# Kernel tuning notes

Measured on AMD Instinct MI355X. Metric: run time of the kernel, lower is better.

Reference implementation:

```python
import jax, jax.numpy as jnp
import numpy as np

B, C, T = 16, 2048, 128      # batch, enc_in (variables), d_model
ID, NC, CD, GD, OUT = 32, 16, 32, 32, 96  # id_dim, num_clusters, cluster_dim, graph_dim, out_len
GIN = T + ID + CD            # gcn_input_dim = 192
NEG = -1.0e9


def setup_inputs() -> dict:
    key = jax.random.key(0)
    ks = jax.random.split(key, 13)
    s = 0.02
    return {
        "x": jax.random.normal(ks[0], (B, C, 1, T), dtype=jnp.float32),
        "id_emb": jax.random.normal(ks[1], (C, ID), dtype=jnp.float32) * s,
        "w1": jax.random.normal(ks[2], (T, T // 2), dtype=jnp.float32) * s,
        "b1": jnp.zeros((T // 2,), dtype=jnp.float32),
        "w2": jax.random.normal(ks[3], (T // 2, ID), dtype=jnp.float32) * s,
        "b2": jnp.zeros((ID,), dtype=jnp.float32),
        "cluster_emb": jax.random.normal(ks[4], (NC, CD), dtype=jnp.float32) * s,
        "wic": jax.random.normal(ks[5], (ID, CD), dtype=jnp.float32) * s,
        "bic": jnp.zeros((CD,), dtype=jnp.float32),
        "wg": jax.random.normal(ks[6], (ID + CD, GD), dtype=jnp.float32) * s,
        "bg": jnp.zeros((GD,), dtype=jnp.float32),
        "context_weight": jax.random.normal(ks[7], (C, GIN), dtype=jnp.float32) * s,
        "wl": jax.random.normal(ks[8], (GIN, OUT), dtype=jnp.float32) * s,
        "bl": jnp.zeros((OUT,), dtype=jnp.float32),
    }


def reference(x, id_emb, w1, b1, w2, b2, cluster_emb, wic, bic, wg, bg,
              context_weight, wl, bl):
    b, c, n, t = x.shape
    xs = x[:, :, 0, :]                                       # [b,c,t] (squeeze dim -2)
    # dynamic id projection: Linear -> ReLU -> Linear
    dyn = jax.nn.relu(xs @ w1 + b1) @ w2 + b2                # [b,c,id]
    id_embeds = id_emb[None, :, :] + dyn                     # static + dynamic
    # soft cluster assignment
    id_for_clustering = id_embeds @ wic + bic                # [b,c,cd]
    probs = jax.nn.softmax(
        jnp.einsum('bcl,nl->bcn', id_for_clustering, cluster_emb), axis=-1)
    cluster_embeds = probs @ cluster_emb                     # [b,c,cd]
    # graph embedding and dynamic dense adjacency
    graph_emb = jnp.concatenate([id_embeds, cluster_embeds], axis=-1) @ wg + bg
    adj = jnp.einsum('bcg,bmg->bcm', graph_emb, graph_emb)   # [b,c,c]
    adj = jax.nn.relu(adj)
    neg = NEG * jnp.eye(c, dtype=adj.dtype)                  # [c,c], -1e9 on diag, 0 off-diag
    adj = adj + neg
    # torch.where(adj<=0, neg_inf_matrix, adj): off-diag nonpositive -> 0, diag -> -1e9
    adj = jnp.where(adj <= 0.0, neg, adj)
    adj = jax.nn.softmax(adj, axis=-1)
    # two-stage GCN aggregation (dropout is identity in eval mode)
    gcn_input = jnp.concatenate([xs, id_embeds, cluster_embeds], axis=-1)  # [b,c,GIN]
    agg = jnp.einsum('boi,bid->bod', adj, gcn_input)         # [b,c,GIN]
    w = jnp.tanh(jnp.einsum('bod,ol->bdl', agg, context_weight))  # [b,GIN,GIN]
    out = (jnp.einsum('bdl,bod->bol', w, gcn_input) + gcn_input) @ wl + bl  # [b,c,out_len]
    return out[:, :, None, :]                                # unsqueeze dim -2
```

## Files before the change

kernel.cpp:

```cpp
#include <hip/hip_runtime.h>
#include <hip/hip_bf16.h>


typedef __attribute__((ext_vector_type(8))) short short8;
typedef __attribute__((ext_vector_type(16))) float f32x16;

__device__ __forceinline__ unsigned short f2bf(float f) {
    __hip_bfloat16 h = __float2bfloat16(f);
    return *reinterpret_cast<unsigned short*>(&h);
}
__device__ __forceinline__ float bf2f(unsigned short u) {
    __hip_bfloat16 h = *reinterpret_cast<__hip_bfloat16*>(&u);
    return __bfloat162float(h);
}

__global__ __launch_bounds__(256) void k0_transpose_x(
    const float* __restrict__ x, unsigned short* __restrict__ vt)
{
    __shared__ float sT[64 * 133];
    const int t = threadIdx.x;
    const int m0 = blockIdx.x * 64;
    const int b = blockIdx.y;
    const float* xb = x + (size_t)b * 2048 * 128;
    #pragma unroll
    for (int kk = 0; kk < 8; ++kk) {
        int i = t + kk * 256;
        int mm = i >> 5, q4 = i & 31;
        float4 v = ((const float4*)(xb + (size_t)(m0 + mm) * 128))[q4];
        float* d = sT + mm * 133 + q4 * 4;
        d[0] = v.x; d[1] = v.y; d[2] = v.z; d[3] = v.w;
    }
    __syncthreads();
    const int mp = t & 31;
    const int ch0 = t >> 5;
    #pragma unroll
    for (int pass = 0; pass < 16; ++pass) {
        int ch = ch0 + pass * 8;
        unsigned int u0 = f2bf(sT[(2 * mp) * 133 + ch]);
        unsigned int u1 = f2bf(sT[(2 * mp + 1) * 133 + ch]);
        *((unsigned int*)(vt + (size_t)(b * 192 + ch) * 2048 + m0) + mp) =
            u0 | (u1 << 16);
    }
}

__global__ __launch_bounds__(256) void k1_tiled(
    const float* __restrict__ x, const float* __restrict__ id_emb,
    const float* __restrict__ w1, const float* __restrict__ b1,
    const float* __restrict__ w2, const float* __restrict__ b2,
    const float* __restrict__ ce, const float* __restrict__ wic,
    const float* __restrict__ bic, const float* __restrict__ wg,
    const float* __restrict__ bg, unsigned short* __restrict__ vt,
    unsigned short* __restrict__ geb16)
{
    __shared__ float sh[32 * 68];
    __shared__ float sid[32 * 36];
    __shared__ float sic[32 * 36];
    __shared__ float scl[32 * 36];
    __shared__ float sp[32 * 20];

    const int t = threadIdx.x;
    const int r0 = blockIdx.x * 32;
    const int b = r0 >> 11;
    const int c0 = r0 & 2047;

    {
        const int row = t >> 3, j0 = (t & 7) * 8;
        const float* xrow = x + (size_t)(r0 + row) * 128;
        float acc[8];
        #pragma unroll
        for (int j = 0; j < 8; ++j) acc[j] = b1[j0 + j];
        float4 pa[4], pb[4];
        float4 pxv;
        #pragma unroll
        for (int u = 0; u < 4; ++u) {
            const float4* wr = (const float4*)(w1 + u * 64 + j0);
            pa[u] = wr[0]; pb[u] = wr[1];
        }
        pxv = *(const float4*)(xrow);
        for (int k0 = 0; k0 < 128; k0 += 4) {
            float4 ca[4], cb[4];
            float4 cxv = pxv;
            #pragma unroll
            for (int u = 0; u < 4; ++u) { ca[u] = pa[u]; cb[u] = pb[u]; }
            const int kn = k0 + 4;
            if (kn < 128) {
                #pragma unroll
                for (int u = 0; u < 4; ++u) {
                    const float4* wr = (const float4*)(w1 + (kn + u) * 64 + j0);
                    pa[u] = wr[0]; pb[u] = wr[1];
                }
                pxv = *(const float4*)(xrow + kn);
            }
            float cx[4] = {cxv.x, cxv.y, cxv.z, cxv.w};
            #pragma unroll
            for (int u = 0; u < 4; ++u) {
                acc[0] = fmaf(cx[u], ca[u].x, acc[0]);
                acc[1] = fmaf(cx[u], ca[u].y, acc[1]);
                acc[2] = fmaf(cx[u], ca[u].z, acc[2]);
                acc[3] = fmaf(cx[u], ca[u].w, acc[3]);
                acc[4] = fmaf(cx[u], cb[u].x, acc[4]);
                acc[5] = fmaf(cx[u], cb[u].y, acc[5]);
                acc[6] = fmaf(cx[u], cb[u].z, acc[6]);
                acc[7] = fmaf(cx[u], cb[u].w, acc[7]);
            }
        }
        float* hr = sh + row * 68 + j0;
        #pragma unroll
        for (int j = 0; j < 8; ++j) hr[j] = fmaxf(acc[j], 0.f);
    }
    __syncthreads();

    {
        const int row = t >> 3, j0 = (t & 7) * 4;
        const int c = c0 + row;
        const float* hrow = sh + row * 68;
        float acc[4];
        #pragma unroll
        for (int j = 0; j < 4; ++j) acc[j] = b2[j0 + j];
        float4 pw[4];
        float  ph[4];
        #pragma unroll
        for (int u = 0; u < 4; ++u) {
            pw[u] = *(const float4*)(w2 + u * 32 + j0);
            ph[u] = hrow[u];
        }
        for (int k0 = 0; k0 < 64; k0 += 4) {
            float4 cw4[4];
            float  ch4[4];
            #pragma unroll
            for (int u = 0; u < 4; ++u) { cw4[u] = pw[u]; ch4[u] = ph[u]; }
            const int kn = k0 + 4;
            if (kn < 64) {
                #pragma unroll
                for (int u = 0; u < 4; ++u) {
                    pw[u] = *(const float4*)(w2 + (kn + u) * 32 + j0);
                    ph[u] = hrow[kn + u];
                }
            }
            #pragma unroll
            for (int u = 0; u < 4; ++u) {
                acc[0] = fmaf(ch4[u], cw4[u].x, acc[0]);
                acc[1] = fmaf(ch4[u], cw4[u].y, acc[1]);
                acc[2] = fmaf(ch4[u], cw4[u].z, acc[2]);
                acc[3] = fmaf(ch4[u], cw4[u].w, acc[3]);
            }
        }
        #pragma unroll
        for (int j = 0; j < 4; ++j) {
            float ide = id_emb[c * 32 + j0 + j] + acc[j];
            sid[row * 36 + j0 + j] = ide;
            vt[(size_t)(b * 192 + 128 + j0 + j) * 2048 + c] = f2bf(ide);
        }
    }
    __syncthreads();

    {
        const int row = t >> 3, j0 = (t & 7) * 4;
        const float* irow = sid + row * 36;
        float acc[4];
        #pragma unroll
        for (int j = 0; j < 4; ++j) acc[j] = bic[j0 + j];
        float4 pw[4];
        float  pi[4];
        #pragma unroll
        for (int u = 0; u < 4; ++u) {
            pw[u] = *(const float4*)(wic + u * 32 + j0);
            pi[u] = irow[u];
        }
        for (int k0 = 0; k0 < 32; k0 += 4) {
            float4 cw4[4];
            float  ci4[4];
            #pragma unroll
            for (int u = 0; u < 4; ++u) { cw4[u] = pw[u]; ci4[u] = pi[u]; }
            const int kn = k0 + 4;
            if (kn < 32) {
                #pragma unroll
                for (int u = 0; u < 4; ++u) {
                    pw[u] = *(const float4*)(wic + (kn + u) * 32 + j0);
                    pi[u] = irow[kn + u];
                }
            }
            #pragma unroll
            for (int u = 0; u < 4; ++u) {
                acc[0] = fmaf(ci4[u], cw4[u].x, acc[0]);
                acc[1] = fmaf(ci4[u], cw4[u].y, acc[1]);
                acc[2] = fmaf(ci4[u], cw4[u].z, acc[2]);
                acc[3] = fmaf(ci4[u], cw4[u].w, acc[3]);
            }
        }
        #pragma unroll
        for (int j = 0; j < 4; ++j) sic[row * 36 + j0 + j] = acc[j];
    }
    __syncthreads();

    {
        const int n = t & 15, rowp = t >> 4;
        const float* cer = ce + n * 32;
        float a0 = 0.f, a1 = 0.f;
        #pragma unroll
        for (int k0 = 0; k0 < 32; k0 += 8) {
            float cv[8], s0[8], s1[8];
            #pragma unroll
            for (int u = 0; u < 8; ++u) {
                cv[u] = cer[k0 + u];
                s0[u] = sic[rowp * 36 + k0 + u];
                s1[u] = sic[(rowp + 16) * 36 + k0 + u];
            }
            #pragma unroll
            for (int u = 0; u < 8; ++u) {
                a0 = fmaf(s0[u], cv[u], a0);
                a1 = fmaf(s1[u], cv[u], a1);
            }
        }
        sp[rowp * 20 + n] = a0;
        sp[(rowp + 16) * 20 + n] = a1;
    }
    __syncthreads();

    if (t < 32) {
        float* pr = sp + t * 20;
        float mx = pr[0];
        for (int n = 1; n < 16; ++n) mx = fmaxf(mx, pr[n]);
        float ss = 0.f;
        for (int n = 0; n < 16; ++n) { float e = __expf(pr[n] - mx); pr[n] = e; ss += e; }
        float inv = 1.f / ss;
        for (int n = 0; n < 16; ++n) pr[n] *= inv;
    }
    __syncthreads();

    {
        const int row = t >> 3, j0 = (t & 7) * 4;
        const int c = c0 + row;
        const float* prow = sp + row * 20;
        float acc[4] = {0.f, 0.f, 0.f, 0.f};
        float4 pc[4];
        float  pp[4];
        #pragma unroll
        for (int u = 0; u < 4; ++u) {
            pc[u] = *(const float4*)(ce + u * 32 + j0);
            pp[u] = prow[u];
        }
        for (int n0 = 0; n0 < 16; n0 += 4) {
            float4 cc4[4];
            float  cp4[4];
            #pragma unroll
            for (int u = 0; u < 4; ++u) { cc4[u] = pc[u]; cp4[u] = pp[u]; }
            const int nn = n0 + 4;
            if (nn < 16) {
                #pragma unroll
                for (int u = 0; u < 4; ++u) {
                    pc[u] = *(const float4*)(ce + (nn + u) * 32 + j0);
                    pp[u] = prow[nn + u];
                }
            }
            #pragma unroll
            for (int u = 0; u < 4; ++u) {
                acc[0] = fmaf(cp4[u], cc4[u].x, acc[0]);
                acc[1] = fmaf(cp4[u], cc4[u].y, acc[1]);
                acc[2] = fmaf(cp4[u], cc4[u].z, acc[2]);
                acc[3] = fmaf(cp4[u], cc4[u].w, acc[3]);
            }
        }
        #pragma unroll
        for (int j = 0; j < 4; ++j) {
            scl[row * 36 + j0 + j] = acc[j];
            vt[(size_t)(b * 192 + 160 + j0 + j) * 2048 + c] = f2bf(acc[j]);
        }
    }
    __syncthreads();

    {
        const int row = t >> 3, j0 = (t & 7) * 4;
        const int r = r0 + row;
        const float* irow = sid + row * 36;
        const float* crow = scl + row * 36;
        float acc[4];
        #pragma unroll
        for (int j = 0; j < 4; ++j) acc[j] = bg[j0 + j];
        {
            float4 pw[4];
            float  pi[4];
            #pragma unroll
            for (int u = 0; u < 4; ++u) {
                pw[u] = *(const float4*)(wg + u * 32 + j0);
                pi[u] = irow[u];
            }
            for (int k0 = 0; k0 < 32; k0 += 4) {
                float4 cw4[4];
                float  ci4[4];
                #pragma unroll
                for (int u = 0; u < 4; ++u) { cw4[u] = pw[u]; ci4[u] = pi[u]; }
                const int kn = k0 + 4;
                if (kn < 32) {
                    #pragma unroll
                    for (int u = 0; u < 4; ++u) {
                        pw[u] = *(const float4*)(wg + (kn + u) * 32 + j0);
                        pi[u] = irow[kn + u];
                    }
                }
                #pragma unroll
                for (int u = 0; u < 4; ++u) {
                    acc[0] = fmaf(ci4[u], cw4[u].x, acc[0]);
                    acc[1] = fmaf(ci4[u], cw4[u].y, acc[1]);
                    acc[2] = fmaf(ci4[u], cw4[u].z, acc[2]);
                    acc[3] = fmaf(ci4[u], cw4[u].w, acc[3]);
                }
            }
        }
        {
            float4 pw[4];
            float  pcv[4];
            #pragma unroll
            for (int u = 0; u < 4; ++u) {
                pw[u] = *(const float4*)(wg + (32 + u) * 32 + j0);
                pcv[u] = crow[u];
            }
            for (int k0 = 0; k0 < 32; k0 += 4) {
                float4 cw4[4];
                float  cc4[4];
                #pragma unroll
                for (int u = 0; u < 4; ++u) { cw4[u] = pw[u]; cc4[u] = pcv[u]; }
                const int kn = k0 + 4;
                if (kn < 32) {
                    #pragma unroll
                    for (int u = 0; u < 4; ++u) {
                        pw[u] = *(const float4*)(wg + (32 + kn + u) * 32 + j0);
                        pcv[u] = crow[kn + u];
                    }
                }
                #pragma unroll
                for (int u = 0; u < 4; ++u) {
                    acc[0] = fmaf(cc4[u], cw4[u].x, acc[0]);
                    acc[1] = fmaf(cc4[u], cw4[u].y, acc[1]);
                    acc[2] = fmaf(cc4[u], cw4[u].z, acc[2]);
                    acc[3] = fmaf(cc4[u], cw4[u].w, acc[3]);
                }
            }
        }
        #pragma unroll
        for (int j = 0; j < 4; ++j)
            geb16[(size_t)r * 32 + j0 + j] = f2bf(acc[j]);
    }
}

__global__ __launch_bounds__(256) void k1b_sumv(
    const unsigned short* __restrict__ vt, float* __restrict__ sumv)
{
    __shared__ float red[256];
    const int ch = blockIdx.x, b = blockIdx.y, t = threadIdx.x;
    const unsigned short* row = vt + (size_t)(b * 192 + ch) * 2048;
    float a = 0.f;
    #pragma unroll
    for (int j = 0; j < 8; ++j) a += bf2f(row[t * 8 + j]);
    red[t] = a; __syncthreads();
    for (int off = 128; off > 0; off >>= 1) {
        if (t < off) red[t] += red[t + off];
        __syncthreads();
    }
    if (t == 0) sumv[b * 192 + ch] = red[0];
}

__global__ __launch_bounds__(256) void k2_fused(
    const unsigned short* __restrict__ geb16,
    const unsigned short* __restrict__ vt,
    const float* __restrict__ sumv,
    unsigned short* __restrict__ aggb)
{
    __shared__ unsigned short sGe[2][64 * 40];
    __shared__ unsigned short sVt[192 * 72];
    __shared__ unsigned short dw[64 * 72];
    __shared__ float s_sum[192];
    __shared__ float sinv[64];
    float* lpbuf = (float*)sVt;

    const int t = threadIdx.x;
    const int lin = blockIdx.x + gridDim.x * blockIdx.y;
    const int nb = (lin & 7) * 64 + (lin >> 3);
    const int o0 = (nb & 31) * 64;
    const int b = nb >> 5;
    const unsigned short* geb = geb16 + (size_t)b * 2048 * 32;
    const unsigned short* vtb = vt + (size_t)b * 192 * 2048;

    const int lane = t & 63;
    const int mg = t >> 6;
    const int col = lane & 31;
    const int grp = lane >> 5;
    const int os = (mg & 1) * 32;
    const int ms = (mg >> 1) * 32;
    const int orow0 = (mg & 1) * 32;
    const int dbase = (mg >> 1) * 96;

    const int ge_row = t >> 2, ge_c8 = t & 3;

    short8 rGe;
    short8 rVt0, rVt1, rVt2, rVt3, rVt4, rVt5;

    if (t < 192) s_sum[t] = sumv[b * 192 + t];

    short8 Areg0 = *(const short8*)(geb + (size_t)(o0 + os + col) * 32 + 0 * 16 + grp * 8);
    short8 Areg1 = *(const short8*)(geb + (size_t)(o0 + os + col) * 32 + 1 * 16 + grp * 8);

    {
        rGe = *(const short8*)(geb + (size_t)ge_row * 32 + ge_c8 * 8);
        int i0;
        i0 = t + 0 * 256; rVt0 = *(const short8*)(vtb + (size_t)(i0 >> 3) * 2048 + 0 + (i0 & 7) * 8);
        i0 = t + 1 * 256; rVt1 = *(const short8*)(vtb + (size_t)(i0 >> 3) * 2048 + 0 + (i0 & 7) * 8);
        i0 = t + 2 * 256; rVt2 = *(const short8*)(vtb + (size_t)(i0 >> 3) * 2048 + 0 + (i0 & 7) * 8);
        i0 = t + 3 * 256; rVt3 = *(const short8*)(vtb + (size_t)(i0 >> 3) * 2048 + 0 + (i0 & 7) * 8);
        i0 = t + 4 * 256; rVt4 = *(const short8*)(vtb + (size_t)(i0 >> 3) * 2048 + 0 + (i0 & 7) * 8);
        i0 = t + 5 * 256; rVt5 = *(const short8*)(vtb + (size_t)(i0 >> 3) * 2048 + 0 + (i0 & 7) * 8);
    }
    {
        *(short8*)(sGe[0] + ge_row * 40 + ge_c8 * 8) = rGe;
        int i0;
        i0 = t + 0 * 256; *(short8*)(sVt + (i0 >> 3) * 72 + (i0 & 7) * 8) = rVt0;
        i0 = t + 1 * 256; *(short8*)(sVt + (i0 >> 3) * 72 + (i0 & 7) * 8) = rVt1;
        i0 = t + 2 * 256; *(short8*)(sVt + (i0 >> 3) * 72 + (i0 & 7) * 8) = rVt2;
        i0 = t + 3 * 256; *(short8*)(sVt + (i0 >> 3) * 72 + (i0 & 7) * 8) = rVt3;
        i0 = t + 4 * 256; *(short8*)(sVt + (i0 >> 3) * 72 + (i0 & 7) * 8) = rVt4;
        i0 = t + 5 * 256; *(short8*)(sVt + (i0 >> 3) * 72 + (i0 & 7) * 8) = rVt5;
    }
    __syncthreads();

    f32x16 acc0, acc1, acc2;
    #pragma unroll
    for (int i = 0; i < 16; ++i) { acc0[i] = 0.f; acc1[i] = 0.f; acc2[i] = 0.f; }
    float lpA[16];
    #pragma unroll
    for (int i = 0; i < 16; ++i) lpA[i] = 0.f;

    int cur = 0;
    for (int m0 = 0; m0 < 2048; m0 += 64) {
        const bool have_next = (m0 + 64 < 2048);

        if (have_next) {
            const int mn = m0 + 64;
            rGe = *(const short8*)(geb + (size_t)(mn + ge_row) * 32 + ge_c8 * 8);
            int i0;
            i0 = t + 0 * 256; rVt0 = *(const short8*)(vtb + (size_t)(i0 >> 3) * 2048 + mn + (i0 & 7) * 8);
            i0 = t + 1 * 256; rVt1 = *(const short8*)(vtb + (size_t)(i0 >> 3) * 2048 + mn + (i0 & 7) * 8);
            i0 = t + 2 * 256; rVt2 = *(const short8*)(vtb + (size_t)(i0 >> 3) * 2048 + mn + (i0 & 7) * 8);
            i0 = t + 3 * 256; rVt3 = *(const short8*)(vtb + (size_t)(i0 >> 3) * 2048 + mn + (i0 & 7) * 8);
            i0 = t + 4 * 256; rVt4 = *(const short8*)(vtb + (size_t)(i0 >> 3) * 2048 + mn + (i0 & 7) * 8);
            i0 = t + 5 * 256; rVt5 = *(const short8*)(vtb + (size_t)(i0 >> 3) * 2048 + mn + (i0 & 7) * 8);
        }

        f32x16 sacc;
        #pragma unroll
        for (int i = 0; i < 16; ++i) sacc[i] = 0.f;
        {
            short8 Bf0 = *(const short8*)(sGe[cur] + (ms + col) * 40 + 0 * 16 + grp * 8);
            short8 Bf1 = *(const short8*)(sGe[cur] + (ms + col) * 40 + 1 * 16 + grp * 8);
            sacc = __builtin_amdgcn_mfma_f32_32x32x16_bf16(Areg0, Bf0, sacc, 0, 0, 0);
            sacc = __builtin_amdgcn_mfma_f32_32x32x16_bf16(Areg1, Bf1, sacc, 0, 0, 0);
        }
        {
            const int m_local = ms + col;
            if (m0 != o0) {
                #pragma unroll
                for (int r = 0; r < 16; ++r) {
                    int o_local = os + (r & 3) + 8 * (r >> 2) + 4 * grp;
                    float s = sacc[r];
                    float d = (s > 0.f) ? (__expf(s) - 1.f) : 0.f;
                    lpA[r] += d;
                    dw[o_local * 72 + m_local] = f2bf(d);
                }
            } else {
                const int gm = m0 + m_local;
                #pragma unroll
                for (int r = 0; r < 16; ++r) {
                    int o_local = os + (r & 3) + 8 * (r >> 2) + 4 * grp;
                    float s = sacc[r];
                    float d = (gm == o0 + o_local) ? -1.f
                            : ((s > 0.f) ? (__expf(s) - 1.f) : 0.f);
                    lpA[r] += d;
                    dw[o_local * 72 + m_local] = f2bf(d);
                }
            }
        }
        if (have_next)
            *(short8*)(sGe[cur ^ 1] + ge_row * 40 + ge_c8 * 8) = rGe;

        __syncthreads();

        #pragma unroll
        for (int ks = 0; ks < 4; ++ks) {
            short8 A  = *(const short8*)(dw + (orow0 + col) * 72 + ks * 16 + grp * 8);
            short8 B0 = *(const short8*)(sVt + (dbase + col) * 72 + ks * 16 + grp * 8);
            short8 B1v = *(const short8*)(sVt + (dbase + 32 + col) * 72 + ks * 16 + grp * 8);
            short8 B2v = *(const short8*)(sVt + (dbase + 64 + col) * 72 + ks * 16 + grp * 8);
            acc0 = __builtin_amdgcn_mfma_f32_32x32x16_bf16(A, B0, acc0, 0, 0, 0);
            acc1 = __builtin_amdgcn_mfma_f32_32x32x16_bf16(A, B1v, acc1, 0, 0, 0);
            acc2 = __builtin_amdgcn_mfma_f32_32x32x16_bf16(A, B2v, acc2, 0, 0, 0);
        }

        __syncthreads();

        if (have_next) {
            int i0;
            i0 = t + 0 * 256; *(short8*)(sVt + (i0 >> 3) * 72 + (i0 & 7) * 8) = rVt0;
            i0 = t + 1 * 256; *(short8*)(sVt + (i0 >> 3) * 72 + (i0 & 7) * 8) = rVt1;
            i0 = t + 2 * 256; *(short8*)(sVt + (i0 >> 3) * 72 + (i0 & 7) * 8) = rVt2;
            i0 = t + 3 * 256; *(short8*)(sVt + (i0 >> 3) * 72 + (i0 & 7) * 8) = rVt3;
            i0 = t + 4 * 256; *(short8*)(sVt + (i0 >> 3) * 72 + (i0 & 7) * 8) = rVt4;
            i0 = t + 5 * 256; *(short8*)(sVt + (i0 >> 3) * 72 + (i0 & 7) * 8) = rVt5;
        }
        cur ^= 1;
    }

    __syncthreads();
    {
        const int widx = mg >> 1;
        #pragma unroll
        for (int r = 0; r < 16; ++r) {
            int ol = os + (r & 3) + 8 * (r >> 2) + 4 * grp;
            lpbuf[(widx * 32 + col) * 68 + ol] = lpA[r];
        }
    }
    __syncthreads();
    if (t < 64) {
        float l = 2048.f;
        for (int i = 0; i < 64; ++i) l += lpbuf[i * 68 + t];
        sinv[t] = 1.f / l;
    }
    __syncthreads();

    {
        f32x16 av[3] = {acc0, acc1, acc2};
        unsigned short* ab = aggb + (size_t)b * 2048 * 192;
        #pragma unroll
        for (int n = 0; n < 3; ++n) {
            int chn = dbase + n * 32 + col;
            float sv = s_sum[chn];
            #pragma unroll
            for (int r = 0; r < 16; ++r) {
                int ol = orow0 + (r & 3) + 8 * (r >> 2) + 4 * grp;
                ab[(size_t)(o0 + ol) * 192 + chn] =
                    f2bf((sv + av[n][r]) * sinv[ol]);
            }
        }
    }
}

__global__ __launch_bounds__(256) void k3a_split(
    const float* __restrict__ cw, unsigned short* __restrict__ cwhi,
    unsigned short* __restrict__ cwlo)
{
    const int idx = blockIdx.x * 256 + threadIdx.x;
    float v = cw[idx];
    unsigned short h = f2bf(v);
    cwhi[idx] = h;
    cwlo[idx] = f2bf(v - bf2f(h));
}

__global__ __launch_bounds__(256) void k3_mfma_sk(
    const unsigned short* __restrict__ aggb,
    const unsigned short* __restrict__ cwhi,
    const unsigned short* __restrict__ cwlo,
    float* __restrict__ wpart)
{
    const int t = threadIdx.x;
    const int slot = blockIdx.z;
    const int b = slot >> 3;
    const int ks = slot & 7;
    const int d0 = blockIdx.x * 64;
    const int l0 = blockIdx.y * 64;
    const unsigned short* ab = aggb + (size_t)b * 2048 * 192;

    const int lane = t & 63;
    const int w = t >> 6;
    const int col = lane & 31;
    const int grp = lane >> 5;
    const int drow = d0 + (w & 1) * 32 + col;
    const int lrow = l0 + (w >> 1) * 32 + col;

    f32x16 acc;
    #pragma unroll
    for (int i = 0; i < 16; ++i) acc[i] = 0.f;

    const int obase = ks * 256;
    #pragma unroll 4
    for (int ostep = 0; ostep < 16; ++ostep) {
        const int ob = obase + ostep * 16 + grp * 8;
        short8 A, Bh, Bl;
        #pragma unroll
        for (int i = 0; i < 8; ++i) {
            const size_t ro = (size_t)(ob + i) * 192;
            A[i]  = (short)ab[ro + drow];
            Bh[i] = (short)cwhi[ro + lrow];
            Bl[i] = (short)cwlo[ro + lrow];
        }
        acc = __builtin_amdgcn_mfma_f32_32x32x16_bf16(A, Bh, acc, 0, 0, 0);
        acc = __builtin_amdgcn_mfma_f32_32x32x16_bf16(A, Bl, acc, 0, 0, 0);
    }

    float* wp = wpart + (size_t)slot * 36864;
    const int lcol = l0 + (w >> 1) * 32 + col;
    #pragma unroll
    for (int r = 0; r < 16; ++r) {
        int dl = d0 + (w & 1) * 32 + (r & 3) + 8 * (r >> 2) + 4 * grp;
        wp[(size_t)dl * 192 + lcol] = acc[r];
    }
}

__global__ __launch_bounds__(256) void k3_ctx_sk(
    const unsigned short* __restrict__ aggb, const float* __restrict__ cw,
    float* __restrict__ wpart)
{
    __shared__ float sA[64 * 68];
    __shared__ float sW[64 * 68];
    const int t = threadIdx.x;
    const int slot = blockIdx.z;
    const int b = slot >> 3;
    const int ks = slot & 7;
    const int d0 = blockIdx.x * 64;
    const int l0 = blockIdx.y * 64;
    const unsigned short* ab = aggb + (size_t)b * 2048 * 192;
    const int ti = t >> 4, tj = t & 15;
    float acc[4][4] = {{0.f}};

    for (int o0 = ks * 256; o0 < ks * 256 + 256; o0 += 64) {
        for (int i = t; i < 4096; i += 256) {
            int oo = i >> 6, dd = i & 63;
            sA[oo * 68 + dd] = bf2f(ab[(size_t)(o0 + oo) * 192 + d0 + dd]);
            sW[oo * 68 + dd] = cw[(size_t)(o0 + oo) * 192 + l0 + dd];
        }
        __syncthreads();
        for (int o = 0; o < 64; ++o) {
            const float* ap = sA + o * 68 + ti * 4;
            const float* wp = sW + o * 68 + tj * 4;
            float a0 = ap[0], a1 = ap[1], a2 = ap[2], a3 = ap[3];
            float w0 = wp[0], w1v = wp[1], w2v = wp[2], w3 = wp[3];
            acc[0][0] = fmaf(a0, w0, acc[0][0]); acc[0][1] = fmaf(a0, w1v, acc[0][1]);
            acc[0][2] = fmaf(a0, w2v, acc[0][2]); acc[0][3] = fmaf(a0, w3, acc[0][3]);
            acc[1][0] = fmaf(a1, w0, acc[1][0]); acc[1][1] = fmaf(a1, w1v, acc[1][1]);
            acc[1][2] = fmaf(a1, w2v, acc[1][2]); acc[1][3] = fmaf(a1, w3, acc[1][3]);
            acc[2][0] = fmaf(a2, w0, acc[2][0]); acc[2][1] = fmaf(a2, w1v, acc[2][1]);
            acc[2][2] = fmaf(a2, w2v, acc[2][2]); acc[2][3] = fmaf(a2, w3, acc[2][3]);
            acc[3][0] = fmaf(a3, w0, acc[3][0]); acc[3][1] = fmaf(a3, w1v, acc[3][1]);
            acc[3][2] = fmaf(a3, w2v, acc[3][2]); acc[3][3] = fmaf(a3, w3, acc[3][3]);
        }
        __syncthreads();
    }
    float* wp = wpart + (size_t)slot * 36864;
    #pragma unroll
    for (int i = 0; i < 4; ++i)
        #pragma unroll
        for (int j = 0; j < 4; ++j)
            wp[(d0 + ti * 4 + i) * 192 + l0 + tj * 4 + j] = acc[i][j];
}

__global__ __launch_bounds__(256) void k3r_reduce(
    const float* __restrict__ wpart, float* __restrict__ wraw)
{
    const int idx = blockIdx.x * 256 + threadIdx.x;
    const int b = blockIdx.y;
    const float* base = wpart + (size_t)b * 8 * 36864 + idx;
    float a = 0.f;
    #pragma unroll
    for (int ks = 0; ks < 8; ++ks) a += base[(size_t)ks * 36864];
    wraw[(size_t)b * 36864 + idx] = tanhf(a);
}

__global__ __launch_bounds__(256) void k3_ctx(
    const unsigned short* __restrict__ aggb, const float* __restrict__ cw,
    float* __restrict__ wraw)
{
    __shared__ float sA[64 * 68];
    __shared__ float sW[64 * 68];
    const int t = threadIdx.x;
    const int b = blockIdx.z;
    const int d0 = blockIdx.x * 64;
    const int l0 = blockIdx.y * 64;
    const unsigned short* ab = aggb + (size_t)b * 2048 * 192;
    const int ti = t >> 4, tj = t & 15;
    float acc[4][4] = {{0.f}};

    for (int o0 = 0; o0 < 2048; o0 += 64) {
        for (int i = t; i < 4096; i += 256) {
            int oo = i >> 6, dd = i & 63;
            sA[oo * 68 + dd] = bf2f(ab[(size_t)(o0 + oo) * 192 + d0 + dd]);
            sW[oo * 68 + dd] = cw[(size_t)(o0 + oo) * 192 + l0 + dd];
        }
        __syncthreads();
        for (int o = 0; o < 64; ++o) {
            const float* ap = sA + o * 68 + ti * 4;
            const float* wp = sW + o * 68 + tj * 4;
            float a0 = ap[0], a1 = ap[1], a2 = ap[2], a3 = ap[3];
            float w0 = wp[0], w1v = wp[1], w2v = wp[2], w3 = wp[3];
            acc[0][0] = fmaf(a0, w0, acc[0][0]); acc[0][1] = fmaf(a0, w1v, acc[0][1]);
            acc[0][2] = fmaf(a0, w2v, acc[0][2]); acc[0][3] = fmaf(a0, w3, acc[0][3]);
            acc[1][0] = fmaf(a1, w0, acc[1][0]); acc[1][1] = fmaf(a1, w1v, acc[1][1]);
            acc[1][2] = fmaf(a1, w2v, acc[1][2]); acc[1][3] = fmaf(a1, w3, acc[1][3]);
            acc[2][0] = fmaf(a2, w0, acc[2][0]); acc[2][1] = fmaf(a2, w1v, acc[2][1]);
            acc[2][2] = fmaf(a2, w2v, acc[2][2]); acc[2][3] = fmaf(a2, w3, acc[2][3]);
            acc[3][0] = fmaf(a3, w0, acc[3][0]); acc[3][1] = fmaf(a3, w1v, acc[3][1]);
            acc[3][2] = fmaf(a3, w2v, acc[3][2]); acc[3][3] = fmaf(a3, w3, acc[3][3]);
        }
        __syncthreads();
    }
    float* wb = wraw + (size_t)b * 36864;
    #pragma unroll
    for (int i = 0; i < 4; ++i)
        #pragma unroll
        for (int j = 0; j < 4; ++j)
            wb[(d0 + ti * 4 + i) * 192 + l0 + tj * 4 + j] = tanhf(acc[i][j]);
}

__global__ __launch_bounds__(192) void k3b_m2(
    const float* __restrict__ wmat, const float* __restrict__ wl,
    float* __restrict__ m2)
{
    const int t = threadIdx.x;
    const int b = blockIdx.y;
    const int d = blockIdx.x * 2 + (t / 96);
    const int l = t % 96;
    const float* wrow = wmat + (size_t)b * 36864 + d * 192;
    float acc = wl[d * 96 + l];
    float pa[8], pb[8];
    #pragma unroll
    for (int u = 0; u < 8; ++u) { pa[u] = wrow[u]; pb[u] = wl[u * 96 + l]; }
    for (int k0 = 0; k0 < 192; k0 += 8) {
        float ca[8], cb[8];
        #pragma unroll
        for (int u = 0; u < 8; ++u) { ca[u] = pa[u]; cb[u] = pb[u]; }
        const int kn = k0 + 8;
        if (kn < 192) {
            #pragma unroll
            for (int u = 0; u < 8; ++u) {
                pa[u] = wrow[kn + u];
                pb[u] = wl[(kn + u) * 96 + l];
            }
        }
        #pragma unroll
        for (int u = 0; u < 8; ++u) acc = fmaf(ca[u], cb[u], acc);
    }
    m2[(size_t)b * 18432 + d * 96 + l] = acc;
}

__global__ __launch_bounds__(192) void k4_tiled(
    const float* __restrict__ x, const unsigned short* __restrict__ vt,
    const float* __restrict__ m2, const float* __restrict__ bl,
    float* __restrict__ out)
{
    __shared__ float sm2[192 * 96];
    const int t = threadIdx.x;
    const int rblk = blockIdx.x;
    const int b = blockIdx.y;
    {
        const float4* src = (const float4*)(m2 + (size_t)b * 18432);
        float4* dst = (float4*)sm2;
        #pragma unroll
        for (int i = 0; i < 24; ++i) dst[t + i * 192] = src[t + i * 192];
    }
    __syncthreads();

    const int rg = t / 12;
    const int cg = t % 12;
    const int j0 = cg * 8;
    const int cloc = rblk * 64 + rg * 4;
    const int rr = b * 2048 + cloc;
    float acc[4][8];
    #pragma unroll
    for (int i = 0; i < 4; ++i)
        #pragma unroll
        for (int j = 0; j < 8; ++j) acc[i][j] = bl[j0 + j];

    for (int k0 = 0; k0 < 128; k0 += 8) {
        float rv[4][8];
        #pragma unroll
        for (int i = 0; i < 4; ++i) {
            const float4* xr = (const float4*)(x + (size_t)(rr + i) * 128 + k0);
            float4 a = xr[0], c4 = xr[1];
            rv[i][0] = a.x; rv[i][1] = a.y; rv[i][2] = a.z; rv[i][3] = a.w;
            rv[i][4] = c4.x; rv[i][5] = c4.y; rv[i][6] = c4.z; rv[i][7] = c4.w;
        }
        #pragma unroll
        for (int kk = 0; kk < 8; ++kk) {
            const float* mr = sm2 + (k0 + kk) * 96 + j0;
            float mv[8];
            #pragma unroll
            for (int j = 0; j < 8; ++j) mv[j] = mr[j];
            #pragma unroll
            for (int i = 0; i < 4; ++i)
                #pragma unroll
                for (int j = 0; j < 8; ++j)
                    acc[i][j] = fmaf(rv[i][kk], mv[j], acc[i][j]);
        }
    }
    for (int k = 128; k < 192; ++k) {
        const unsigned short* vr = vt + (size_t)(b * 192 + k) * 2048 + cloc;
        float rv0 = bf2f(vr[0]), rv1 = bf2f(vr[1]);
        float rv2 = bf2f(vr[2]), rv3 = bf2f(vr[3]);
        const float* mr = sm2 + k * 96 + j0;
        #pragma unroll
        for (int j = 0; j < 8; ++j) {
            float mv = mr[j];
            acc[0][j] = fmaf(rv0, mv, acc[0][j]);
            acc[1][j] = fmaf(rv1, mv, acc[1][j]);
            acc[2][j] = fmaf(rv2, mv, acc[2][j]);
            acc[3][j] = fmaf(rv3, mv, acc[3][j]);
        }
    }
    #pragma unroll
    for (int i = 0; i < 4; ++i) {
        float* orow = out + (size_t)(rr + i) * 96 + j0;
        *(float4*)orow = make_float4(acc[i][0], acc[i][1], acc[i][2], acc[i][3]);
        *(float4*)(orow + 4) = make_float4(acc[i][4], acc[i][5], acc[i][6], acc[i][7]);
    }
}

extern "C" void kernel_launch(void* const* d_in, const int* in_sizes, int n_in,
                              void* d_out, int out_size, void* d_ws, size_t ws_size,
                              hipStream_t stream) {
    const float* x      = (const float*)d_in[0];
    const float* id_emb = (const float*)d_in[1];
    const float* w1     = (const float*)d_in[2];
    const float* b1     = (const float*)d_in[3];
    const float* w2     = (const float*)d_in[4];
    const float* b2     = (const float*)d_in[5];
    const float* ce     = (const float*)d_in[6];
    const float* wic    = (const float*)d_in[7];
    const float* bic    = (const float*)d_in[8];
    const float* wg     = (const float*)d_in[9];
    const float* bg     = (const float*)d_in[10];
    const float* cw     = (const float*)d_in[11];
    const float* wl     = (const float*)d_in[12];
    const float* bl     = (const float*)d_in[13];
    float* out = (float*)d_out;

    float* ws = (float*)d_ws;
    unsigned short* vt    = (unsigned short*)ws;
    unsigned short* geb16 = (unsigned short*)(ws + 3145728);
    unsigned short* aggb  = (unsigned short*)(ws + 3670016);
    float* wraw  = ws + 6815744;
    float* m2    = ws + 7405568;
    float* sumv  = ws + 7700480;
    float* wpart = ws + 7703552;
    unsigned short* cwhi = (unsigned short*)(ws + 12422144);
    unsigned short* cwlo = cwhi + 393216;
    const size_t need_sk   = (7703552ull + 4718592ull) * 4ull;
    const size_t need_mfma = (7703552ull + 4718592ull + 393216ull) * 4ull;
    const bool use_mfma = (ws_size >= need_mfma);
    const bool use_sk   = (ws_size >= need_sk);

    hipLaunchKernelGGL(k0_transpose_x, dim3(32, 16), dim3(256), 0, stream, x, vt);
    hipLaunchKernelGGL(k1_tiled, dim3(1024), dim3(256), 0, stream,
                       x, id_emb, w1, b1, w2, b2, ce, wic, bic, wg, bg, vt, geb16);
    hipLaunchKernelGGL(k1b_sumv, dim3(192, 16), dim3(256), 0, stream, vt, sumv);
    hipLaunchKernelGGL(k2_fused, dim3(32, 16), dim3(256), 0, stream,
                       geb16, vt, sumv, aggb);
    if (use_mfma) {
        hipLaunchKernelGGL(k3a_split, dim3(1536), dim3(256), 0, stream,
                           cw, cwhi, cwlo);
        hipLaunchKernelGGL(k3_mfma_sk, dim3(3, 3, 128), dim3(256), 0, stream,
                           aggb, cwhi, cwlo, wpart);
        hipLaunchKernelGGL(k3r_reduce, dim3(144, 16), dim3(256), 0, stream,
                           wpart, wraw);
    } else if (use_sk) {
        hipLaunchKernelGGL(k3_ctx_sk, dim3(3, 3, 128), dim3(256), 0, stream,
                           aggb, cw, wpart);
        hipLaunchKernelGGL(k3r_reduce, dim3(144, 16), dim3(256), 0, stream,
                           wpart, wraw);
    } else {
        hipLaunchKernelGGL(k3_ctx, dim3(3, 3, 16), dim3(256), 0, stream,
                           aggb, cw, wraw);
    }
    hipLaunchKernelGGL(k3b_m2, dim3(96, 16), dim3(192), 0, stream,
                       wraw, wl, m2);
    hipLaunchKernelGGL(k4_tiled, dim3(32, 16), dim3(192), 0, stream,
                       x, vt, m2, bl, out);
}
```

Baseline: 276.6 us.

## Warp-specialize k2_fused into loader and MFMA roles with double-buffered V tiles

Doubles the k2_fused block to 512 threads. The first 256 threads compute the score MFMA, the exp weights and the aggregation MFMA. The second 256 threads prefetch the next geb and vt tiles from global memory and store them into a second LDS buffer for vt. This takes global loads and LDS stores off the compute warps' critical path so they overlap with the MFMA work. In exchange, LDS use per block roughly doubles for the vt tiles, and half the threads sit idle during compute, which may lower occupancy.

```diff
diff --git a/kernel.cpp b/kernel.cpp
--- a/kernel.cpp
+++ b/kernel.cpp
@@ -360,20 +360,23 @@
     if (t == 0) sumv[b * 192 + ch] = red[0];
 }
 
-__global__ __launch_bounds__(256) void k2_fused(
+__global__ __launch_bounds__(512, 4) void k2_fused(
     const unsigned short* __restrict__ geb16,
     const unsigned short* __restrict__ vt,
     const float* __restrict__ sumv,
     unsigned short* __restrict__ aggb)
 {
     __shared__ unsigned short sGe[2][64 * 40];
-    __shared__ unsigned short sVt[192 * 72];
+    __shared__ unsigned short sVtA[2][192 * 72];
     __shared__ unsigned short dw[64 * 72];
     __shared__ float s_sum[192];
     __shared__ float sinv[64];
-    float* lpbuf = (float*)sVt;
+    float* lpbuf = (float*)sVtA;
 
     const int t = threadIdx.x;
+    const int tc = t & 255;
+    const int role = t >> 8;
+
     const int lin = blockIdx.x + gridDim.x * blockIdx.y;
     const int nb = (lin & 7) * 64 + (lin >> 3);
     const int o0 = (nb & 31) * 64;
@@ -381,8 +384,8 @@
     const unsigned short* geb = geb16 + (size_t)b * 2048 * 32;
     const unsigned short* vtb = vt + (size_t)b * 192 * 2048;
 
-    const int lane = t & 63;
-    const int mg = t >> 6;
+    const int lane = tc & 63;
+    const int mg = tc >> 6;
     const int col = lane & 31;
     const int grp = lane >> 5;
     const int os = (mg & 1) * 32;
@@ -390,35 +393,32 @@
     const int orow0 = (mg & 1) * 32;
     const int dbase = (mg >> 1) * 96;
 
-    const int ge_row = t >> 2, ge_c8 = t & 3;
-
-    short8 rGe;
-    short8 rVt0, rVt1, rVt2, rVt3, rVt4, rVt5;
+    const int ge_row = tc >> 2, ge_c8 = tc & 3;
 
     if (t < 192) s_sum[t] = sumv[b * 192 + t];
 
-    short8 Areg0 = *(const short8*)(geb + (size_t)(o0 + os + col) * 32 + 0 * 16 + grp * 8);
-    short8 Areg1 = *(const short8*)(geb + (size_t)(o0 + os + col) * 32 + 1 * 16 + grp * 8);
-
-    {
+    short8 Areg0, Areg1;
+    short8 rGe, rVt0, rVt1, rVt2, rVt3, rVt4, rVt5;
+
+    if (role == 0) {
+        Areg0 = *(const short8*)(geb + (size_t)(o0 + os + col) * 32 + 0 * 16 + grp * 8);
+        Areg1 = *(const short8*)(geb + (size_t)(o0 + os + col) * 32 + 1 * 16 + grp * 8);
+    } else {
         rGe = *(const short8*)(geb + (size_t)ge_row * 32 + ge_c8 * 8);
         int i0;
-        i0 = t + 0 * 256; rVt0 = *(const short8*)(vtb + (size_t)(i0 >> 3) * 2048 + 0 + (i0 & 7) * 8);
-        i0 = t + 1 * 256; rVt1 = *(const short8*)(vtb + (size_t)(i0 >> 3) * 2048 + 0 + (i0 & 7) * 8);
-        i0 = t + 2 * 256; rVt2 = *(const short8*)(vtb + (size_t)(i0 >> 3) * 2048 + 0 + (i0 & 7) * 8);
-        i0 = t + 3 * 256; rVt3 = *(const short8*)(vtb + (size_t)(i0 >> 3) * 2048 + 0 + (i0 & 7) * 8);
-        i0 = t + 4 * 256; rVt4 = *(const short8*)(vtb + (size_t)(i0 >> 3) * 2048 + 0 + (i0 & 7) * 8);
-        i0 = t + 5 * 256; rVt5 = *(const short8*)(vtb + (size_t)(i0 >> 3) * 2048 + 0 + (i0 & 7) * 8);
-    }
-    {
+        i0 = tc + 0 * 256; rVt0 = *(const short8*)(vtb + (size_t)(i0 >> 3) * 2048 + 0 + (i0 & 7) * 8);
+        i0 = tc + 1 * 256; rVt1 = *(const short8*)(vtb + (size_t)(i0 >> 3) * 2048 + 0 + (i0 & 7) * 8);
+        i0 = tc + 2 * 256; rVt2 = *(const short8*)(vtb + (size_t)(i0 >> 3) * 2048 + 0 + (i0 & 7) * 8);
+        i0 = tc + 3 * 256; rVt3 = *(const short8*)(vtb + (size_t)(i0 >> 3) * 2048 + 0 + (i0 & 7) * 8);
+        i0 = tc + 4 * 256; rVt4 = *(const short8*)(vtb + (size_t)(i0 >> 3) * 2048 + 0 + (i0 & 7) * 8);
+        i0 = tc + 5 * 256; rVt5 = *(const short8*)(vtb + (size_t)(i0 >> 3) * 2048 + 0 + (i0 & 7) * 8);
         *(short8*)(sGe[0] + ge_row * 40 + ge_c8 * 8) = rGe;
-        int i0;
-        i0 = t + 0 * 256; *(short8*)(sVt + (i0 >> 3) * 72 + (i0 & 7) * 8) = rVt0;
-        i0 = t + 1 * 256; *(short8*)(sVt + (i0 >> 3) * 72 + (i0 & 7) * 8) = rVt1;
-        i0 = t + 2 * 256; *(short8*)(sVt + (i0 >> 3) * 72 + (i0 & 7) * 8) = rVt2;
-        i0 = t + 3 * 256; *(short8*)(sVt + (i0 >> 3) * 72 + (i0 & 7) * 8) = rVt3;
-        i0 = t + 4 * 256; *(short8*)(sVt + (i0 >> 3) * 72 + (i0 & 7) * 8) = rVt4;
-        i0 = t + 5 * 256; *(short8*)(sVt + (i0 >> 3) * 72 + (i0 & 7) * 8) = rVt5;
+        i0 = tc + 0 * 256; *(short8*)(sVtA[0] + (i0 >> 3) * 72 + (i0 & 7) * 8) = rVt0;
+        i0 = tc + 1 * 256; *(short8*)(sVtA[0] + (i0 >> 3) * 72 + (i0 & 7) * 8) = rVt1;
+        i0 = tc + 2 * 256; *(short8*)(sVtA[0] + (i0 >> 3) * 72 + (i0 & 7) * 8) = rVt2;
+        i0 = tc + 3 * 256; *(short8*)(sVtA[0] + (i0 >> 3) * 72 + (i0 & 7) * 8) = rVt3;
+        i0 = tc + 4 * 256; *(short8*)(sVtA[0] + (i0 >> 3) * 72 + (i0 & 7) * 8) = rVt4;
+        i0 = tc + 5 * 256; *(short8*)(sVtA[0] + (i0 >> 3) * 72 + (i0 & 7) * 8) = rVt5;
     }
     __syncthreads();
 
@@ -433,28 +433,28 @@
     for (int m0 = 0; m0 < 2048; m0 += 64) {
         const bool have_next = (m0 + 64 < 2048);
 
-        if (have_next) {
-            const int mn = m0 + 64;
-            rGe = *(const short8*)(geb + (size_t)(mn + ge_row) * 32 + ge_c8 * 8);
-            int i0;
-            i0 = t + 0 * 256; rVt0 = *(const short8*)(vtb + (size_t)(i0 >> 3) * 2048 + mn + (i0 & 7) * 8);
-            i0 = t + 1 * 256; rVt1 = *(const short8*)(vtb + (size_t)(i0 >> 3) * 2048 + mn + (i0 & 7) * 8);
-            i0 = t + 2 * 256; rVt2 = *(const short8*)(vtb + (size_t)(i0 >> 3) * 2048 + mn + (i0 & 7) * 8);
-            i0 = t + 3 * 256; rVt3 = *(const short8*)(vtb + (size_t)(i0 >> 3) * 2048 + mn + (i0 & 7) * 8);
-            i0 = t + 4 * 256; rVt4 = *(const short8*)(vtb + (size_t)(i0 >> 3) * 2048 + mn + (i0 & 7) * 8);
-            i0 = t + 5 * 256; rVt5 = *(const short8*)(vtb + (size_t)(i0 >> 3) * 2048 + mn + (i0 & 7) * 8);
-        }
-
-        f32x16 sacc;
-        #pragma unroll
-        for (int i = 0; i < 16; ++i) sacc[i] = 0.f;
-        {
-            short8 Bf0 = *(const short8*)(sGe[cur] + (ms + col) * 40 + 0 * 16 + grp * 8);
-            short8 Bf1 = *(const short8*)(sGe[cur] + (ms + col) * 40 + 1 * 16 + grp * 8);
-            sacc = __builtin_amdgcn_mfma_f32_32x32x16_bf16(Areg0, Bf0, sacc, 0, 0, 0);
-            sacc = __builtin_amdgcn_mfma_f32_32x32x16_bf16(Areg1, Bf1, sacc, 0, 0, 0);
-        }
-        {
+        if (role == 1) {
+            if (have_next) {
+                const int mn = m0 + 64;
+                rGe = *(const short8*)(geb + (size_t)(mn + ge_row) * 32 + ge_c8 * 8);
+                int i0;
+                i0 = tc + 0 * 256; rVt0 = *(const short8*)(vtb + (size_t)(i0 >> 3) * 2048 + mn + (i0 & 7) * 8);
+                i0 = tc + 1 * 256; rVt1 = *(const short8*)(vtb + (size_t)(i0 >> 3) * 2048 + mn + (i0 & 7) * 8);
+                i0 = tc + 2 * 256; rVt2 = *(const short8*)(vtb + (size_t)(i0 >> 3) * 2048 + mn + (i0 & 7) * 8);
+                i0 = tc + 3 * 256; rVt3 = *(const short8*)(vtb + (size_t)(i0 >> 3) * 2048 + mn + (i0 & 7) * 8);
+                i0 = tc + 4 * 256; rVt4 = *(const short8*)(vtb + (size_t)(i0 >> 3) * 2048 + mn + (i0 & 7) * 8);
+                i0 = tc + 5 * 256; rVt5 = *(const short8*)(vtb + (size_t)(i0 >> 3) * 2048 + mn + (i0 & 7) * 8);
+            }
+        } else {
+            f32x16 sacc;
+            #pragma unroll
+            for (int i = 0; i < 16; ++i) sacc[i] = 0.f;
+            {
+                short8 Bf0 = *(const short8*)(sGe[cur] + (ms + col) * 40 + 0 * 16 + grp * 8);
+                short8 Bf1 = *(const short8*)(sGe[cur] + (ms + col) * 40 + 1 * 16 + grp * 8);
+                sacc = __builtin_amdgcn_mfma_f32_32x32x16_bf16(Areg0, Bf0, sacc, 0, 0, 0);
+                sacc = __builtin_amdgcn_mfma_f32_32x32x16_bf16(Areg1, Bf1, sacc, 0, 0, 0);
+            }
             const int m_local = ms + col;
             if (m0 != o0) {
                 #pragma unroll
@@ -478,38 +478,37 @@
                 }
             }
         }
-        if (have_next)
-            *(short8*)(sGe[cur ^ 1] + ge_row * 40 + ge_c8 * 8) = rGe;
 
         __syncthreads();
 
-        #pragma unroll
-        for (int ks = 0; ks < 4; ++ks) {
-            short8 A  = *(const short8*)(dw + (orow0 + col) * 72 + ks * 16 + grp * 8);
-            short8 B0 = *(const short8*)(sVt + (dbase + col) * 72 + ks * 16 + grp * 8);
-            short8 B1v = *(const short8*)(sVt + (dbase + 32 + col) * 72 + ks * 16 + grp * 8);
-            short8 B2v = *(const short8*)(sVt + (dbase + 64 + col) * 72 + ks * 16 + grp * 8);
-            acc0 = __builtin_amdgcn_mfma_f32_32x32x16_bf16(A, B0, acc0, 0, 0, 0);
-            acc1 = __builtin_amdgcn_mfma_f32_32x32x16_bf16(A, B1v, acc1, 0, 0, 0);
-            acc2 = __builtin_amdgcn_mfma_f32_32x32x16_bf16(A, B2v, acc2, 0, 0, 0);
+        if (role == 0) {
+            #pragma unroll
+            for (int ks = 0; ks < 4; ++ks) {
+                short8 A   = *(const short8*)(dw + (orow0 + col) * 72 + ks * 16 + grp * 8);
+                short8 B0v = *(const short8*)(sVtA[cur] + (dbase + col) * 72 + ks * 16 + grp * 8);
+                short8 B1v = *(const short8*)(sVtA[cur] + (dbase + 32 + col) * 72 + ks * 16 + grp * 8);
+                short8 B2v = *(const short8*)(sVtA[cur] + (dbase + 64 + col) * 72 + ks * 16 + grp * 8);
+                acc0 = __builtin_amdgcn_mfma_f32_32x32x16_bf16(A, B0v, acc0, 0, 0, 0);
+                acc1 = __builtin_amdgcn_mfma_f32_32x32x16_bf16(A, B1v, acc1, 0, 0, 0);
+                acc2 = __builtin_amdgcn_mfma_f32_32x32x16_bf16(A, B2v, acc2, 0, 0, 0);
+            }
+        } else if (have_next) {
+            const int nbuf = cur ^ 1;
+            *(short8*)(sGe[nbuf] + ge_row * 40 + ge_c8 * 8) = rGe;
+            int i0;
+            i0 = tc + 0 * 256; *(short8*)(sVtA[nbuf] + (i0 >> 3) * 72 + (i0 & 7) * 8) = rVt0;
+            i0 = tc + 1 * 256; *(short8*)(sVtA[nbuf] + (i0 >> 3) * 72 + (i0 & 7) * 8) = rVt1;
+            i0 = tc + 2 * 256; *(short8*)(sVtA[nbuf] + (i0 >> 3) * 72 + (i0 & 7) * 8) = rVt2;
+            i0 = tc + 3 * 256; *(short8*)(sVtA[nbuf] + (i0 >> 3) * 72 + (i0 & 7) * 8) = rVt3;
+            i0 = tc + 4 * 256; *(short8*)(sVtA[nbuf] + (i0 >> 3) * 72 + (i0 & 7) * 8) = rVt4;
+            i0 = tc + 5 * 256; *(short8*)(sVtA[nbuf] + (i0 >> 3) * 72 + (i0 & 7) * 8) = rVt5;
         }
 
         __syncthreads();
-
-        if (have_next) {
-            int i0;
-            i0 = t + 0 * 256; *(short8*)(sVt + (i0 >> 3) * 72 + (i0 & 7) * 8) = rVt0;
-            i0 = t + 1 * 256; *(short8*)(sVt + (i0 >> 3) * 72 + (i0 & 7) * 8) = rVt1;
-            i0 = t + 2 * 256; *(short8*)(sVt + (i0 >> 3) * 72 + (i0 & 7) * 8) = rVt2;
-            i0 = t + 3 * 256; *(short8*)(sVt + (i0 >> 3) * 72 + (i0 & 7) * 8) = rVt3;
-            i0 = t + 4 * 256; *(short8*)(sVt + (i0 >> 3) * 72 + (i0 & 7) * 8) = rVt4;
-            i0 = t + 5 * 256; *(short8*)(sVt + (i0 >> 3) * 72 + (i0 & 7) * 8) = rVt5;
-        }
         cur ^= 1;
     }
 
-    __syncthreads();
-    {
+    if (role == 0) {
         const int widx = mg >> 1;
         #pragma unroll
         for (int r = 0; r < 16; ++r) {
@@ -525,7 +524,7 @@
     }
     __syncthreads();
 
-    {
+    if (role == 0) {
         f32x16 av[3] = {acc0, acc1, acc2};
         unsigned short* ab = aggb + (size_t)b * 2048 * 192;
         #pragma unroll
@@ -848,7 +847,7 @@
     hipLaunchKernelGGL(k1_tiled, dim3(1024), dim3(256), 0, stream,
                        x, id_emb, w1, b1, w2, b2, ce, wic, bic, wg, bg, vt, geb16);
     hipLaunchKernelGGL(k1b_sumv, dim3(192, 16), dim3(256), 0, stream, vt, sumv);
-    hipLaunchKernelGGL(k2_fused, dim3(32, 16), dim3(256), 0, stream,
+    hipLaunchKernelGGL(k2_fused, dim3(32, 16), dim3(512), 0, stream,
                        geb16, vt, sumv, aggb);
     if (use_mfma) {
         hipLaunchKernelGGL(k3a_split, dim3(1536), dim3(256), 0, stream,
```

Measured after the change: 339.2 us. 22.6% more time.
